# Performance work log

Measured on AMD Instinct MI355X. Metric: run time of the kernel, lower is better.

Reference implementation:

```python
import jax, jax.numpy as jnp
import numpy as np

NB_HEAD = 16
SIZE_PER_HEAD = 64
D_MODEL = NB_HEAD * SIZE_PER_HEAD  # 1024
B, S = 4, 2048
NEG_BIG = 1e10


def setup_inputs() -> dict:
    key = jax.random.key(0)
    ks = jax.random.split(key, 9)
    glorot = lambda k, shape: jax.random.uniform(
        k, shape, jnp.float32, -1.0, 1.0) * np.sqrt(6.0 / (shape[0] + shape[1]))
    return {
        "Q_emb": jax.random.normal(ks[0], (B, S, D_MODEL), jnp.float32),
        "K_emb": jax.random.normal(ks[1], (B, S, D_MODEL), jnp.float32),
        "V_emb": jax.random.normal(ks[2], (B, S, D_MODEL), jnp.float32),
        "Q_ini": jax.random.randint(ks[3], (B, S), 0, 50),
        "K_ini": jax.random.randint(ks[4], (B, S), 0, 50),
        "WQ": glorot(ks[5], (D_MODEL, D_MODEL)),
        "WK": glorot(ks[6], (D_MODEL, D_MODEL)),
        "WV": glorot(ks[7], (D_MODEL, D_MODEL)),
        "WO": glorot(ks[8], (D_MODEL, D_MODEL)),
    }


def _proj(x, W):
    # [B,S,D] @ [D, H*dh] -> [B,H,S,dh]
    b, s, _ = x.shape
    y = jnp.einsum('bsd,de->bse', x, W)
    return y.reshape(b, s, NB_HEAD, SIZE_PER_HEAD).transpose(0, 2, 1, 3)


def reference(Q_emb, K_emb, V_emb, Q_ini, K_ini, WQ, WK, WV, WO):
    b, sq, _ = Q_emb.shape
    sk = K_emb.shape[1]
    q = _proj(Q_emb, WQ)
    k = _proj(K_emb, WK)
    v = _proj(V_emb, WV)
    scores = jnp.einsum('bhqd,bhkd->bhqk', q, k) / jnp.sqrt(
        jnp.asarray(SIZE_PER_HEAD, scores_dtype := q.dtype))
    # pad mask: 1 where key token id != 0, broadcast over queries
    pad = (K_ini != 0).astype(scores.dtype)[:, None, None, :]  # [B,1,1,Sk]
    # sub mask: cumsum of eye along rows == lower-triangular causal mask
    causal = jnp.tril(jnp.ones((sq, sk), scores.dtype))[None, None]  # [1,1,Sq,Sk]
    mask = jnp.minimum(pad, causal)
    scores = scores - (1.0 - mask) * NEG_BIG
    attn = jax.nn.softmax(scores, axis=-1)
    ctx = jnp.einsum('bhqk,bhkd->bhqd', attn, v)
    ctx = ctx.transpose(0, 2, 1, 3).reshape(b, sq, NB_HEAD * SIZE_PER_HEAD)
    return jnp.einsum('bsd,de->bse', ctx, WO)
```

## Files before the change

### kernel.cpp

```cpp
#include <hip/hip_runtime.h>

typedef __bf16 bf16_t;
typedef __bf16 bf16x8 __attribute__((ext_vector_type(8)));
typedef __bf16 bf16x4 __attribute__((ext_vector_type(4)));
typedef float  f32x4  __attribute__((ext_vector_type(4)));

#define S_LEN 2048
#define NH    16
#define DH    64
#define DM    1024
#define BATCH 4
#define LOG2E 1.44269504088896f
#define NEGB  (-1.44269504e10f)

static __device__ __forceinline__ f32x4 mfma16(bf16x8 a, bf16x8 b, f32x4 c) {
    return __builtin_amdgcn_mfma_f32_16x16x32_bf16(a, b, c, 0, 0, 0);
}

#if __has_builtin(__builtin_amdgcn_exp2f)
static __device__ __forceinline__ float exp2_hw(float x) {
    return __builtin_amdgcn_exp2f(x);
}
#else
static __device__ __forceinline__ float exp2_hw(float x) {
    float r;
    asm("v_exp_f32 %0, %1" : "=v"(r) : "v"(x));
    return r;
}
#endif

static __device__ __forceinline__ void gl_lds16(const bf16_t* g, bf16_t* l) {
    __builtin_amdgcn_global_load_lds(
        (const __attribute__((address_space(1))) unsigned int*)g,
        (__attribute__((address_space(3))) unsigned int*)l, 16, 0, 0);
}

__global__ __launch_bounds__(256) void cvt3_bf16(const float* __restrict__ s0,
                                                 const float* __restrict__ s1,
                                                 const float* __restrict__ s2,
                                                 bf16_t* __restrict__ d0,
                                                 bf16_t* __restrict__ d1,
                                                 bf16_t* __restrict__ d2, int n) {
    int z = blockIdx.y;
    const float* s = (z == 0) ? s0 : (z == 1) ? s1 : s2;
    bf16_t*      d = (z == 0) ? d0 : (z == 1) ? d1 : d2;
    int i = (blockIdx.x * 256 + threadIdx.x) * 8;
    if (i >= n) return;
    const float4* q = (const float4*)(s + i);
    float4 a = q[0], b = q[1];
    bf16x8 r;
    r[0] = (bf16_t)a.x; r[1] = (bf16_t)a.y; r[2] = (bf16_t)a.z; r[3] = (bf16_t)a.w;
    r[4] = (bf16_t)b.x; r[5] = (bf16_t)b.y; r[6] = (bf16_t)b.z; r[7] = (bf16_t)b.w;
    *(bf16x8*)(d + i) = r;
}

__global__ __launch_bounds__(256) void wtrans(const float* __restrict__ W,
                                              bf16_t* __restrict__ Wt, float scale) {
    __shared__ bf16_t tile[32][33];
    int x = threadIdx.x, ty = threadIdx.y;
    int bx = blockIdx.x * 32, by = blockIdx.y * 32;
#pragma unroll
    for (int i = 0; i < 4; ++i) {
        int y = ty * 4 + i;
        tile[y][x] = (bf16_t)(W[(by + y) * DM + bx + x] * scale);
    }
    __syncthreads();
#pragma unroll
    for (int i = 0; i < 4; ++i) {
        int y = ty * 4 + i;
        Wt[(bx + y) * DM + by + x] = tile[x][y];
    }
}

__global__ __launch_bounds__(256) void btrans(const bf16_t* __restrict__ src,
                                              bf16_t* __restrict__ dst,
                                              int R, int C) {
    __shared__ bf16_t tile[32][33];
    int x = threadIdx.x, ty = threadIdx.y;
    int bx = blockIdx.x * 32, by = blockIdx.y * 32;
#pragma unroll
    for (int i = 0; i < 4; ++i) {
        int y = ty * 4 + i;
        tile[y][x] = src[(size_t)(by + y) * C + bx + x];
    }
    __syncthreads();
#pragma unroll
    for (int i = 0; i < 4; ++i) {
        int y = ty * 4 + i;
        dst[(size_t)(bx + y) * R + by + x] = tile[x][y];
    }
}

template <typename CT>
__global__ __launch_bounds__(512) void gemm_nt_256(const bf16_t* __restrict__ A,
                                                   const bf16_t* __restrict__ Bt,
                                                   CT* __restrict__ C,
                                                   int M, int N, int K, float alpha,
                                                   size_t zsA, size_t zsB, size_t zsC) {
    __shared__ __align__(16) bf16_t As[2 * 256 * 32];
    __shared__ __align__(16) bf16_t Bs[2 * 128 * 32];
    A  += (size_t)blockIdx.z * zsA;
    Bt += (size_t)blockIdx.z * zsB;
    C  += (size_t)blockIdx.z * zsC;
    int tid = threadIdx.x, wave = tid >> 6, lane = tid & 63;
    int l15 = lane & 15, quad = lane >> 4;
    int wm = wave >> 1, wn = wave & 1;
    int bm = blockIdx.x * 256, bn = blockIdx.y * 128;
    int srow = lane >> 2, skx = (lane & 3) << 3;

    f32x4 acc[4][4] = {};

    for (int k0 = 0; k0 < K; k0 += 64) {
#pragma unroll
        for (int c = 0; c < 4; ++c) {
            int t = wave * 4 + c;
            int kk = t & 1, rb = (t >> 1) * 16;
            gl_lds16(A + (size_t)(bm + rb + srow) * K + k0 + kk * 32 + skx,
                     As + kk * 8192 + rb * 32);
        }
#pragma unroll
        for (int c = 0; c < 2; ++c) {
            int t = wave * 2 + c;
            int kk = t & 1, rb = (t >> 1) * 16;
            gl_lds16(Bt + (size_t)(bn + rb + srow) * K + k0 + kk * 32 + skx,
                     Bs + kk * 4096 + rb * 32);
        }
        __syncthreads();

#pragma unroll
        for (int kk = 0; kk < 2; ++kk) {
            bf16x8 af[4], bfr[4];
#pragma unroll
            for (int i = 0; i < 4; ++i)
                af[i] = *(const bf16x8*)(As + kk * 8192 +
                                         (wm * 64 + i * 16 + l15) * 32 + quad * 8);
#pragma unroll
            for (int j = 0; j < 4; ++j)
                bfr[j] = *(const bf16x8*)(Bs + kk * 4096 +
                                          (wn * 64 + j * 16 + l15) * 32 + quad * 8);
#pragma unroll
            for (int i = 0; i < 4; ++i)
#pragma unroll
                for (int j = 0; j < 4; ++j)
                    acc[i][j] = mfma16(af[i], bfr[j], acc[i][j]);
        }
        __syncthreads();
    }

#pragma unroll
    for (int i = 0; i < 4; ++i)
#pragma unroll
        for (int r = 0; r < 4; ++r) {
            int row = bm + wm * 64 + i * 16 + quad * 4 + r;
#pragma unroll
            for (int j = 0; j < 4; ++j)
                C[(size_t)row * N + bn + wn * 64 + j * 16 + l15] =
                    (CT)(acc[i][j][r] * alpha);
        }
}

__global__ __launch_bounds__(256) void vmean_kernel(const bf16_t* __restrict__ Vp,
                                                    float* __restrict__ Vm) {
    __shared__ float red[4][64];
    int z = blockIdx.y;
    int c = blockIdx.x * 64 + (threadIdx.x & 63);
    int rg = threadIdx.x >> 6;
    const bf16_t* p = Vp + (size_t)z * S_LEN * DM + (size_t)rg * (S_LEN / 4) * DM + c;
    float s = 0.f;
    for (int r = 0; r < S_LEN / 4; ++r) s += (float)p[(size_t)r * DM];
    red[rg][threadIdx.x & 63] = s;
    __syncthreads();
    if (threadIdx.x < 64) {
        float t = red[0][threadIdx.x] + red[1][threadIdx.x] +
                  red[2][threadIdx.x] + red[3][threadIdx.x];
        Vm[z * DM + blockIdx.x * 64 + threadIdx.x] = t * (1.0f / S_LEN);
    }
}

__global__ __launch_bounds__(256, 4) void attn_kernel(const bf16_t* __restrict__ Qp,
                                                      const bf16_t* __restrict__ Kp,
                                                      const bf16_t* __restrict__ VT,
                                                      const int* __restrict__ Kini,
                                                      const float* __restrict__ Vmean,
                                                      bf16_t* __restrict__ ctx,
                                                      int ldv, int nqt) {
    __shared__ __align__(16) bf16_t Ks[64 * 72];
    __shared__ __align__(16) bf16_t VsT[64 * 72];
    __shared__ __align__(16) bf16_t Ps[4][16 * 72];
    __shared__ bf16_t padb[2048];

    int bid = blockIdx.x;
    int qt = nqt - 1 - (bid >> 6);
    int hz = bid & 63;
    int h = hz & 15, z = hz >> 4;
    int tid = threadIdx.x, wave = tid >> 6, lane = tid & 63;
    int l15 = lane & 15, quad = lane >> 4;
    int qb0 = qt * 128 + wave * 32;
    size_t rowz = (size_t)z * S_LEN;
    int ntiles = 2 * qt + 2;
    int nkeys = ntiles * 64;

    for (int i = tid; i < nkeys; i += 256)
        padb[i] = (Kini[rowz + i] == 0) ? (bf16_t)NEGB : (bf16_t)(0.0f);

    const bf16_t* qptr = Qp + (rowz + qb0 + l15) * DM + h * DH + quad * 8;
    bf16x8 qa00 = *(const bf16x8*)qptr;
    bf16x8 qa01 = *(const bf16x8*)(qptr + 32);
    bf16x8 qa10 = *(const bf16x8*)(qptr + 16 * DM);
    bf16x8 qa11 = *(const bf16x8*)(qptr + 16 * DM + 32);

    f32x4 o0[4] = {}, o1[4] = {};
    f32x4 l40 = {0.f,0.f,0.f,0.f}, l41 = {0.f,0.f,0.f,0.f};
    int q0 = qb0 + l15, q1 = q0 + 16;
    int q0max = qb0 + 15, q1max = qb0 + 31;

    int srow = tid >> 2, sch = (tid & 3) << 4;
    const bf16_t* kgb = Kp + (rowz + srow) * DM + h * DH + sch;
    const bf16_t* vgb = VT + (size_t)(h * DH + srow) * ldv + rowz + sch;

    bf16x8 kr0 = *(const bf16x8*)kgb,        kr1 = *(const bf16x8*)(kgb + 8);
    bf16x8 vr0 = *(const bf16x8*)vgb,        vr1 = *(const bf16x8*)(vgb + 8);

    for (int kt = 0; kt < ntiles; ++kt) {
        int kb = kt * 64;
        *(bf16x8*)(Ks  + srow * 72 + sch)     = kr0;
        *(bf16x8*)(Ks  + srow * 72 + sch + 8) = kr1;
        *(bf16x8*)(VsT + srow * 72 + sch)     = vr0;
        *(bf16x8*)(VsT + srow * 72 + sch + 8) = vr1;
        __syncthreads();

        int nkb = (kt + 1 < ntiles) ? kb + 64 : kb;
        const bf16_t* kg = kgb + (size_t)nkb * DM;
        const bf16_t* vg = vgb + nkb;
        kr0 = *(const bf16x8*)kg; kr1 = *(const bf16x8*)(kg + 8);
        vr0 = *(const bf16x8*)vg; vr1 = *(const bf16x8*)(vg + 8);

        if (kb <= q1max) {
            bool live0 = (kb <= q0max);
            bool bnd = (kb + 63 > qb0);
            f32x4 s1[4];
#pragma unroll
            for (int ks = 0; ks < 4; ++ks) {
                bf16x8 kf0 = *(const bf16x8*)(Ks + (ks * 16 + l15) * 72 + quad * 8);
                bf16x8 kf1 = *(const bf16x8*)(Ks + (ks * 16 + l15) * 72 + 32 + quad * 8);
                bf16x4 pb = *(const bf16x4*)(padb + kb + ks * 16 + quad * 4);
                f32x4 t1 = {0.f, 0.f, 0.f, 0.f};
                t1 = mfma16(kf0, qa10, t1);
                t1 = mfma16(kf1, qa11, t1);
#pragma unroll
                for (int r = 0; r < 4; ++r) t1[r] += (float)pb[r];
                if (bnd) {
#pragma unroll
                    for (int r = 0; r < 4; ++r)
                        if (kb + ks * 16 + quad * 4 + r > q1) t1[r] = NEGB;
                }
                s1[ks] = t1;
                if (live0) {
                    f32x4 t0 = {0.f, 0.f, 0.f, 0.f};
                    t0 = mfma16(kf0, qa00, t0);
                    t0 = mfma16(kf1, qa01, t0);
#pragma unroll
                    for (int r = 0; r < 4; ++r) t0[r] += (float)pb[r];
                    if (bnd) {
#pragma unroll
                        for (int r = 0; r < 4; ++r)
                            if (kb + ks * 16 + quad * 4 + r > q0) t0[r] = NEGB;
                    }
#pragma unroll
                    for (int r = 0; r < 4; ++r) t0[r] = exp2_hw(t0[r]);
                    l40 += t0;
                    bf16x4 pk;
#pragma unroll
                    for (int r = 0; r < 4; ++r) pk[r] = (bf16_t)t0[r];
                    *(bf16x4*)(Ps[wave] + l15 * 72 + ks * 16 + quad * 4) = pk;
                }
            }
            bf16x8 pa00, pa01;
            if (live0) {
                pa00 = *(const bf16x8*)(Ps[wave] + l15 * 72 + quad * 8);
                pa01 = *(const bf16x8*)(Ps[wave] + l15 * 72 + 32 + quad * 8);
            }
#pragma unroll
            for (int ks = 0; ks < 4; ++ks) {
                f32x4 t1 = s1[ks];
#pragma unroll
                for (int r = 0; r < 4; ++r) t1[r] = exp2_hw(t1[r]);
                l41 += t1;
                bf16x4 pk;
#pragma unroll
                for (int r = 0; r < 4; ++r) pk[r] = (bf16_t)t1[r];
                *(bf16x4*)(Ps[wave] + l15 * 72 + ks * 16 + quad * 4) = pk;
            }
            bf16x8 pa10 = *(const bf16x8*)(Ps[wave] + l15 * 72 + quad * 8);
            bf16x8 pa11 = *(const bf16x8*)(Ps[wave] + l15 * 72 + 32 + quad * 8);
#pragma unroll
            for (int j = 0; j < 4; ++j) {
                bf16x8 vb0 = *(const bf16x8*)(VsT + (j * 16 + l15) * 72 + quad * 8);
                bf16x8 vb1 = *(const bf16x8*)(VsT + (j * 16 + l15) * 72 + 32 + quad * 8);
                o1[j] = mfma16(vb0, pa10, o1[j]);
                o1[j] = mfma16(vb1, pa11, o1[j]);
                if (live0) {
                    o0[j] = mfma16(vb0, pa00, o0[j]);
                    o0[j] = mfma16(vb1, pa01, o0[j]);
                }
            }
        }
        __syncthreads();
    }

    const float* vm = Vmean + z * DM + h * DH;
    int rr = lane >> 2, cc = (lane & 3) * 16;
#pragma unroll
    for (int u = 0; u < 2; ++u) {
        f32x4 l4 = u ? l41 : l40;
        float l_ = (l4[0] + l4[1]) + (l4[2] + l4[3]);
        l_ += __shfl_xor(l_, 16);
        l_ += __shfl_xor(l_, 32);
        float inv = 1.0f / l_;
        bool dead = (l_ == 0.0f);
#pragma unroll
        for (int j = 0; j < 4; ++j) {
            f32x4 oj = u ? o1[j] : o0[j];
            bf16x4 c;
#pragma unroll
            for (int r = 0; r < 4; ++r) {
                float val = dead ? vm[j * 16 + quad * 4 + r] : oj[r] * inv;
                c[r] = (bf16_t)val;
            }
            *(bf16x4*)(Ps[wave] + l15 * 72 + j * 16 + quad * 4) = c;
        }
        bf16x8 t0 = *(const bf16x8*)(Ps[wave] + rr * 72 + cc);
        bf16x8 t1 = *(const bf16x8*)(Ps[wave] + rr * 72 + cc + 8);
        bf16_t* cp = ctx + (rowz + qb0 + u * 16 + rr) * DM + h * DH + cc;
        *(bf16x8*)cp = t0;
        *(bf16x8*)(cp + 8) = t1;
    }
}

extern "C" void kernel_launch(void* const* d_in, const int* in_sizes, int n_in,
                              void* d_out, int out_size, void* d_ws, size_t ws_size,
                              hipStream_t stream) {
    const float* Qe = (const float*)d_in[0];
    const float* Ke = (const float*)d_in[1];
    const float* Ve = (const float*)d_in[2];
    const int* Kini = (const int*)d_in[4];
    const float* WQ = (const float*)d_in[5];
    const float* WK = (const float*)d_in[6];
    const float* WV = (const float*)d_in[7];
    const float* WO = (const float*)d_in[8];
    float* out = (float*)d_out;

    const size_t EMB = (size_t)BATCH * S_LEN * DM;
    const size_t SB  = (size_t)S_LEN * DM;
    const size_t WSZ = (size_t)DM * DM;
    const size_t need_full = (6 * EMB + 4 * WSZ) * sizeof(bf16_t)
                           + (size_t)BATCH * DM * sizeof(float);

    dim3 tb32(32, 8), tg32(32, 32);
    const float qscale = 0.125f * LOG2E;

    if (ws_size >= need_full) {
        bf16_t* Qb  = (bf16_t*)d_ws;
        bf16_t* Kb  = Qb + EMB;
        bf16_t* Vb  = Kb + EMB;
        bf16_t* WQt = Vb + EMB;
        bf16_t* WKt = WQt + WSZ;
        bf16_t* WVt = WKt + WSZ;
        bf16_t* WOt = WVt + WSZ;
        bf16_t* Qp  = WOt + WSZ;
        bf16_t* Kp  = Qp + EMB;
        bf16_t* Vp  = Kp + EMB;
        float*  Vm  = (float*)(Vp + EMB);
        bf16_t* Cx  = Qp;
        bf16_t* VT  = Vb;

        int cg = (int)(EMB / (8 * 256));
        cvt3_bf16<<<dim3(cg, 3), 256, 0, stream>>>(Qe, Ke, Ve, Qb, Kb, Vb, (int)EMB);
        wtrans<<<tg32, tb32, 0, stream>>>(WQ, WQt, qscale);
        wtrans<<<tg32, tb32, 0, stream>>>(WK, WKt, 1.0f);
        wtrans<<<tg32, tb32, 0, stream>>>(WV, WVt, 1.0f);
        wtrans<<<tg32, tb32, 0, stream>>>(WO, WOt, 1.0f);

        gemm_nt_256<bf16_t><<<dim3(8192 / 256, DM / 128, 3), 512, 0, stream>>>(
            Qb, WQt, Qp, 8192, DM, DM, 1.0f, EMB, WSZ, EMB);

        btrans<<<dim3(DM / 32, 8192 / 32), tb32, 0, stream>>>(Vp, VT, 8192, DM);
        vmean_kernel<<<dim3(DM / 64, BATCH), 256, 0, stream>>>(Vp, Vm);
        attn_kernel<<<dim3((S_LEN / 128) * NH * BATCH), 256, 0, stream>>>(
            Qp, Kp, VT, Kini, Vm, Cx, 8192, S_LEN / 128);

        gemm_nt_256<float><<<dim3(8192 / 256, DM / 128, 1), 512, 0, stream>>>(
            Cx, WOt, out, 8192, DM, DM, 1.0f, 0, 0, 0);
    } else {
        bf16_t* Qb  = (bf16_t*)d_ws;
        bf16_t* Kb  = Qb + SB;
        bf16_t* Vb  = Kb + SB;
        bf16_t* WQt = Vb + SB;
        bf16_t* WKt = WQt + WSZ;
        bf16_t* WVt = WKt + WSZ;
        bf16_t* WOt = WVt + WSZ;
        bf16_t* Qp  = WOt + WSZ;
        bf16_t* Kp  = Qp + SB;
        bf16_t* Vp  = Kp + SB;
        float*  Vm  = (float*)(Vp + SB);
        bf16_t* Cx  = Qp;
        bf16_t* VT  = Vb;

        wtrans<<<tg32, tb32, 0, stream>>>(WQ, WQt, qscale);
        wtrans<<<tg32, tb32, 0, stream>>>(WK, WKt, 1.0f);
        wtrans<<<tg32, tb32, 0, stream>>>(WV, WVt, 1.0f);
        wtrans<<<tg32, tb32, 0, stream>>>(WO, WOt, 1.0f);

        int cg = (int)(SB / (8 * 256));
        for (int b = 0; b < BATCH; ++b) {
            const size_t off = (size_t)b * SB;
            cvt3_bf16<<<dim3(cg, 3), 256, 0, stream>>>(
                Qe + off, Ke + off, Ve + off, Qb, Kb, Vb, (int)SB);
            gemm_nt_256<bf16_t><<<dim3(2048 / 256, DM / 128, 3), 512, 0, stream>>>(
                Qb, WQt, Qp, 2048, DM, DM, 1.0f, SB, WSZ, SB);
            btrans<<<dim3(DM / 32, 2048 / 32), tb32, 0, stream>>>(Vp, VT, 2048, DM);
            vmean_kernel<<<dim3(DM / 64, 1), 256, 0, stream>>>(Vp, Vm);
            attn_kernel<<<dim3((S_LEN / 128) * NH), 256, 0, stream>>>(
                Qp, Kp, VT, Kini + (size_t)b * S_LEN, Vm, Cx, 2048, S_LEN / 128);
            gemm_nt_256<float><<<dim3(2048 / 256, DM / 128, 1), 512, 0, stream>>>(
                Cx, WOt, out + off, 2048, DM, DM, 1.0f, 0, 0, 0);
        }
    }
}
```

Before: 352.5 us.

## Load K/V fragments directly from global memory, dropping shared-memory staging and barriers

Removes the shared-memory K and V tiles and the register prefetch pipeline. Each wave now reads its MFMA operands straight from global memory (relying on L1/L2) and runs only the key tiles it needs, so the per-tile __syncthreads go away. Launch bounds drop from 4 to 3 blocks per CU. The cost is that the four waves fetch the same K/V data redundantly, there is no software prefetch to hide global latency, and occupancy may be lower.

After: 422.1 us. 1.2x slower.

```diff
diff --git a/kernel.cpp b/kernel.cpp
--- a/kernel.cpp
+++ b/kernel.cpp
@@ -177,15 +177,13 @@
     }
 }
 
-__global__ __launch_bounds__(256, 4) void attn_kernel(const bf16_t* __restrict__ Qp,
+__global__ __launch_bounds__(256, 3) void attn_kernel(const bf16_t* __restrict__ Qp,
                                                       const bf16_t* __restrict__ Kp,
                                                       const bf16_t* __restrict__ VT,
                                                       const int* __restrict__ Kini,
                                                       const float* __restrict__ Vmean,
                                                       bf16_t* __restrict__ ctx,
                                                       int ldv, int nqt) {
-    __shared__ __align__(16) bf16_t Ks[64 * 72];
-    __shared__ __align__(16) bf16_t VsT[64 * 72];
     __shared__ __align__(16) bf16_t Ps[4][16 * 72];
     __shared__ bf16_t padb[2048];
 
@@ -197,11 +195,11 @@
     int l15 = lane & 15, quad = lane >> 4;
     int qb0 = qt * 128 + wave * 32;
     size_t rowz = (size_t)z * S_LEN;
-    int ntiles = 2 * qt + 2;
-    int nkeys = ntiles * 64;
+    int nkeys = (qt + 1) * 128;
 
     for (int i = tid; i < nkeys; i += 256)
         padb[i] = (Kini[rowz + i] == 0) ? (bf16_t)NEGB : (bf16_t)(0.0f);
+    __syncthreads();
 
     const bf16_t* qptr = Qp + (rowz + qb0 + l15) * DM + h * DH + quad * 8;
     bf16x8 qa00 = *(const bf16x8*)qptr;
@@ -214,98 +212,82 @@
     int q0 = qb0 + l15, q1 = q0 + 16;
     int q0max = qb0 + 15, q1max = qb0 + 31;
 
-    int srow = tid >> 2, sch = (tid & 3) << 4;
-    const bf16_t* kgb = Kp + (rowz + srow) * DM + h * DH + sch;
-    const bf16_t* vgb = VT + (size_t)(h * DH + srow) * ldv + rowz + sch;
-
-    bf16x8 kr0 = *(const bf16x8*)kgb,        kr1 = *(const bf16x8*)(kgb + 8);
-    bf16x8 vr0 = *(const bf16x8*)vgb,        vr1 = *(const bf16x8*)(vgb + 8);
-
-    for (int kt = 0; kt < ntiles; ++kt) {
+    const bf16_t* kbase = Kp + (rowz)*DM + h * DH;
+    const bf16_t* vbase = VT + (size_t)(h * DH) * ldv + rowz;
+
+    int wnt = (q1max >> 6) + 1;
+    for (int kt = 0; kt < wnt; ++kt) {
         int kb = kt * 64;
-        *(bf16x8*)(Ks  + srow * 72 + sch)     = kr0;
-        *(bf16x8*)(Ks  + srow * 72 + sch + 8) = kr1;
-        *(bf16x8*)(VsT + srow * 72 + sch)     = vr0;
-        *(bf16x8*)(VsT + srow * 72 + sch + 8) = vr1;
-        __syncthreads();
-
-        int nkb = (kt + 1 < ntiles) ? kb + 64 : kb;
-        const bf16_t* kg = kgb + (size_t)nkb * DM;
-        const bf16_t* vg = vgb + nkb;
-        kr0 = *(const bf16x8*)kg; kr1 = *(const bf16x8*)(kg + 8);
-        vr0 = *(const bf16x8*)vg; vr1 = *(const bf16x8*)(vg + 8);
-
-        if (kb <= q1max) {
-            bool live0 = (kb <= q0max);
-            bool bnd = (kb + 63 > qb0);
-            f32x4 s1[4];
-#pragma unroll
-            for (int ks = 0; ks < 4; ++ks) {
-                bf16x8 kf0 = *(const bf16x8*)(Ks + (ks * 16 + l15) * 72 + quad * 8);
-                bf16x8 kf1 = *(const bf16x8*)(Ks + (ks * 16 + l15) * 72 + 32 + quad * 8);
-                bf16x4 pb = *(const bf16x4*)(padb + kb + ks * 16 + quad * 4);
-                f32x4 t1 = {0.f, 0.f, 0.f, 0.f};
-                t1 = mfma16(kf0, qa10, t1);
-                t1 = mfma16(kf1, qa11, t1);
-#pragma unroll
-                for (int r = 0; r < 4; ++r) t1[r] += (float)pb[r];
+        bool live0 = (kb <= q0max);
+        bool bnd = (kb + 63 > qb0);
+        f32x4 s1[4];
+#pragma unroll
+        for (int ks = 0; ks < 4; ++ks) {
+            const bf16_t* kp = kbase + (size_t)(kb + ks * 16 + l15) * DM + quad * 8;
+            bf16x8 kf0 = *(const bf16x8*)kp;
+            bf16x8 kf1 = *(const bf16x8*)(kp + 32);
+            bf16x4 pb = *(const bf16x4*)(padb + kb + ks * 16 + quad * 4);
+            f32x4 t1 = {0.f, 0.f, 0.f, 0.f};
+            t1 = mfma16(kf0, qa10, t1);
+            t1 = mfma16(kf1, qa11, t1);
+#pragma unroll
+            for (int r = 0; r < 4; ++r) t1[r] += (float)pb[r];
+            if (bnd) {
+#pragma unroll
+                for (int r = 0; r < 4; ++r)
+                    if (kb + ks * 16 + quad * 4 + r > q1) t1[r] = NEGB;
+            }
+            s1[ks] = t1;
+            if (live0) {
+                f32x4 t0 = {0.f, 0.f, 0.f, 0.f};
+                t0 = mfma16(kf0, qa00, t0);
+                t0 = mfma16(kf1, qa01, t0);
+#pragma unroll
+                for (int r = 0; r < 4; ++r) t0[r] += (float)pb[r];
                 if (bnd) {
 #pragma unroll
                     for (int r = 0; r < 4; ++r)
-                        if (kb + ks * 16 + quad * 4 + r > q1) t1[r] = NEGB;
+                        if (kb + ks * 16 + quad * 4 + r > q0) t0[r] = NEGB;
                 }
-                s1[ks] = t1;
-                if (live0) {
-                    f32x4 t0 = {0.f, 0.f, 0.f, 0.f};
-                    t0 = mfma16(kf0, qa00, t0);
-                    t0 = mfma16(kf1, qa01, t0);
-#pragma unroll
-                    for (int r = 0; r < 4; ++r) t0[r] += (float)pb[r];
-                    if (bnd) {
-#pragma unroll
-                        for (int r = 0; r < 4; ++r)
-                            if (kb + ks * 16 + quad * 4 + r > q0) t0[r] = NEGB;
-                    }
-#pragma unroll
-                    for (int r = 0; r < 4; ++r) t0[r] = exp2_hw(t0[r]);
-                    l40 += t0;
-                    bf16x4 pk;
-#pragma unroll
-                    for (int r = 0; r < 4; ++r) pk[r] = (bf16_t)t0[r];
-                    *(bf16x4*)(Ps[wave] + l15 * 72 + ks * 16 + quad * 4) = pk;
-                }
-            }
-            bf16x8 pa00, pa01;
-            if (live0) {
-                pa00 = *(const bf16x8*)(Ps[wave] + l15 * 72 + quad * 8);
-                pa01 = *(const bf16x8*)(Ps[wave] + l15 * 72 + 32 + quad * 8);
-            }
-#pragma unroll
-            for (int ks = 0; ks < 4; ++ks) {
-                f32x4 t1 = s1[ks];
-#pragma unroll
-                for (int r = 0; r < 4; ++r) t1[r] = exp2_hw(t1[r]);
-                l41 += t1;
+#pragma unroll
+                for (int r = 0; r < 4; ++r) t0[r] = exp2_hw(t0[r]);
+                l40 += t0;
                 bf16x4 pk;
 #pragma unroll
-                for (int r = 0; r < 4; ++r) pk[r] = (bf16_t)t1[r];
+                for (int r = 0; r < 4; ++r) pk[r] = (bf16_t)t0[r];
                 *(bf16x4*)(Ps[wave] + l15 * 72 + ks * 16 + quad * 4) = pk;
             }
-            bf16x8 pa10 = *(const bf16x8*)(Ps[wave] + l15 * 72 + quad * 8);
-            bf16x8 pa11 = *(const bf16x8*)(Ps[wave] + l15 * 72 + 32 + quad * 8);
-#pragma unroll
-            for (int j = 0; j < 4; ++j) {
-                bf16x8 vb0 = *(const bf16x8*)(VsT + (j * 16 + l15) * 72 + quad * 8);
-                bf16x8 vb1 = *(const bf16x8*)(VsT + (j * 16 + l15) * 72 + 32 + quad * 8);
-                o1[j] = mfma16(vb0, pa10, o1[j]);
-                o1[j] = mfma16(vb1, pa11, o1[j]);
-                if (live0) {
-                    o0[j] = mfma16(vb0, pa00, o0[j]);
-                    o0[j] = mfma16(vb1, pa01, o0[j]);
-                }
+        }
+        bf16x8 pa00, pa01;
+        if (live0) {
+            pa00 = *(const bf16x8*)(Ps[wave] + l15 * 72 + quad * 8);
+            pa01 = *(const bf16x8*)(Ps[wave] + l15 * 72 + 32 + quad * 8);
+        }
+#pragma unroll
+        for (int ks = 0; ks < 4; ++ks) {
+            f32x4 t1 = s1[ks];
+#pragma unroll
+            for (int r = 0; r < 4; ++r) t1[r] = exp2_hw(t1[r]);
+            l41 += t1;
+            bf16x4 pk;
+#pragma unroll
+            for (int r = 0; r < 4; ++r) pk[r] = (bf16_t)t1[r];
+            *(bf16x4*)(Ps[wave] + l15 * 72 + ks * 16 + quad * 4) = pk;
+        }
+        bf16x8 pa10 = *(const bf16x8*)(Ps[wave] + l15 * 72 + quad * 8);
+        bf16x8 pa11 = *(const bf16x8*)(Ps[wave] + l15 * 72 + 32 + quad * 8);
+#pragma unroll
+        for (int j = 0; j < 4; ++j) {
+            const bf16_t* vp = vbase + (size_t)(j * 16 + l15) * ldv + kb + quad * 8;
+            bf16x8 vb0 = *(const bf16x8*)vp;
+            bf16x8 vb1 = *(const bf16x8*)(vp + 32);
+            o1[j] = mfma16(vb0, pa10, o1[j]);
+            o1[j] = mfma16(vb1, pa11, o1[j]);
+            if (live0) {
+                o0[j] = mfma16(vb0, pa00, o0[j]);
+                o0[j] = mfma16(vb1, pa01, o0[j]);
             }
         }
-        __syncthreads();
     }
 
     const float* vm = Vmean + z * DM + h * DH;
```
